# Kernel tuning notes

Hardware: AMD Instinct MI355X
Metric: run time of the kernel (lower is better)

Reference implementation:

```python
import jax, jax.numpy as jnp
import numpy as np

# geomloss SamplesLoss defaults for loss='sinkhorn'
BLUR = 0.05
SCALING = 0.5
P = 1  # norm=1 -> cost C(x,y) = ||x - y||_2


def _cost(x, y):
    # Euclidean distance cost (p=1). x:(B,N,D), y:(B,M,D) -> (B,N,M)
    d2 = (jnp.sum(x * x, -1)[:, :, None]
          - 2.0 * jnp.einsum('bnd,bmd->bnm', x, y)
          + jnp.sum(y * y, -1)[:, None, :])
    return jnp.sqrt(jnp.clip(d2, 1e-12, None))  # tiny clamp keeps sqrt grad finite on diagonal


def _softmin(eps, C, h):
    # f_i = -eps * logsumexp_j( h_j - C_ij / eps );  C:(B,N,M), h:(B,M) -> (B,N)
    return -eps * jax.nn.logsumexp(h[:, None, :] - C / eps, axis=2)


def _eps_schedule(diameter):
    # geomloss epsilon_schedule(p, diameter, blur, scaling)
    return ([diameter ** P]
            + [float(np.exp(e)) for e in np.arange(P * np.log(diameter), P * np.log(BLUR), P * np.log(SCALING))]
            + [BLUR ** P])


def _sinkhorn_divergence(x, y):
    # Debiased Sinkhorn divergence (geomloss, tensorized backend, balanced OT).
    B, N, D = x.shape
    M = y.shape[1]
    a_log = jnp.full((B, N), -np.log(N), dtype=x.dtype)  # uniform weights (log)
    b_log = jnp.full((B, M), -np.log(M), dtype=x.dtype)

    C_xy = _cost(x, y)
    C_yx = jnp.swapaxes(C_xy, 1, 2)  # symmetric cost
    C_xx = _cost(x, x)
    C_yy = _cost(y, y)

    # diameter of the joint point cloud (geomloss max_diameter); concrete python float
    xf = np.asarray(x).reshape(-1, D)
    yf = np.asarray(y).reshape(-1, D)
    mins = np.minimum(xf.min(0), yf.min(0))
    maxs = np.maximum(xf.max(0), yf.max(0))
    diameter = float(np.linalg.norm(maxs - mins))
    eps_list = _eps_schedule(diameter)

    sg = jax.lax.stop_gradient

    # initialization at the largest eps
    eps = eps_list[0]
    f_aa = _softmin(eps, C_xx, a_log)
    g_bb = _softmin(eps, C_yy, b_log)
    g_ab = _softmin(eps, C_yx, a_log)
    f_ba = _softmin(eps, C_xy, b_log)

    # epsilon-annealing loop with symmetric (averaged) updates; no grad flows
    # through this loop (outputs are stop_gradient'ed in the final extrapolation)
    for eps in eps_list:
        ft_ba = _softmin(eps, C_xy, b_log + g_ab / eps)
        gt_ab = _softmin(eps, C_yx, a_log + f_ba / eps)
        f_ba = 0.5 * (f_ba + ft_ba)
        g_ab = 0.5 * (g_ab + gt_ab)
        ft_aa = _softmin(eps, C_xx, a_log + f_aa / eps)
        gt_bb = _softmin(eps, C_yy, b_log + g_bb / eps)
        f_aa = 0.5 * (f_aa + ft_aa)
        g_bb = 0.5 * (g_bb + gt_bb)

    # last extrapolation at eps = blur^p with detached dual potentials (envelope theorem)
    eps = eps_list[-1]
    f_ba_new = _softmin(eps, C_xy, sg(b_log + g_ab / eps))
    g_ab_new = _softmin(eps, C_yx, sg(a_log + f_ba / eps))
    f_aa = _softmin(eps, C_xx, sg(a_log + f_aa / eps))
    g_bb = _softmin(eps, C_yy, sg(b_log + g_bb / eps))
    f_ba, g_ab = f_ba_new, g_ab_new

    a = jnp.exp(a_log)
    b = jnp.exp(b_log)
    # S_eps(a,b) = <a, f_ba - f_aa> + <b, g_ab - g_bb>, per batch element
    return jnp.sum(a * (f_ba - f_aa), -1) + jnp.sum(b * (g_ab - g_bb), -1)


def setup_inputs() -> dict:
    key = jax.random.key(0)
    k1, k2 = jax.random.split(key)
    pre = jax.random.normal(k1, (2, 4096, 2), dtype=jnp.float32)
    gt = jax.random.normal(k2, (2, 4096, 2), dtype=jnp.float32)
    return {"pre": pre, "gt": gt}


def reference(pre, gt):
    return _sinkhorn_divergence(pre, gt).mean()
```

## Files before the change

kernel.cpp:

```cpp
#include <hip/hip_runtime.h>
#include <math.h>

#define NPTS 4096
#define NB 2
#define K_TOTAL 12
#define BLOCK 256
#define TILE 128
#define NT (NPTS / TILE)

#define SCHED_OFF 0
#define ML_OFF 32
#define P_OFF 576
#define POT_SZ (4 * NB * NPTS)
#define PART_OFF (P_OFF + 2 * POT_SZ)
#define PART_SZ (4 * NB * NT * NPTS)

#if __has_builtin(__builtin_amdgcn_exp2f)
#define EXP2F __builtin_amdgcn_exp2f
#else
#define EXP2F exp2f
#endif
#if __has_builtin(__builtin_amdgcn_logf)
#define LOG2F __builtin_amdgcn_logf
#else
#define LOG2F log2f
#endif
#if __has_builtin(__builtin_amdgcn_sqrtf)
#define FSQRTF __builtin_amdgcn_sqrtf
#else
#define FSQRTF sqrtf
#endif

#define BASE_LOGW -8.31776616671934f
#define LOG2E 1.4426950408889634f
#define LN2 0.69314718055994531f

typedef float v2f __attribute__((ext_vector_type(2)));

__global__ __launch_bounds__(BLOCK) void k_init(
    const float2* __restrict__ x, const float2* __restrict__ y, float* ws)
{
  const int tid = threadIdx.x;
  const int bid = blockIdx.x;

  if (bid > 0) {
    for (int i = (bid - 1) * BLOCK + tid; i < 2 * POT_SZ; i += 63 * BLOCK)
      ws[P_OFF + i] = 0.0f;
    return;
  }

  float mnx = 1e30f, mny = 1e30f, mxx = -1e30f, mxy = -1e30f;
  for (int i = tid; i < NB * NPTS; i += BLOCK) {
    float2 p = x[i];
    mnx = fminf(mnx, p.x); mxx = fmaxf(mxx, p.x);
    mny = fminf(mny, p.y); mxy = fmaxf(mxy, p.y);
    float2 q = y[i];
    mnx = fminf(mnx, q.x); mxx = fmaxf(mxx, q.x);
    mny = fminf(mny, q.y); mxy = fmaxf(mxy, q.y);
  }
  for (int o = 32; o; o >>= 1) {
    mnx = fminf(mnx, __shfl_xor(mnx, o, 64));
    mxx = fmaxf(mxx, __shfl_xor(mxx, o, 64));
    mny = fminf(mny, __shfl_xor(mny, o, 64));
    mxy = fmaxf(mxy, __shfl_xor(mxy, o, 64));
  }
  __shared__ float r[4][4];
  const int wave = tid >> 6, lane = tid & 63;
  if (lane == 0) { r[0][wave] = mnx; r[1][wave] = mxx; r[2][wave] = mny; r[3][wave] = mxy; }
  __syncthreads();
  if (tid == 0) {
    mnx = fminf(fminf(r[0][0], r[0][1]), fminf(r[0][2], r[0][3]));
    mxx = fmaxf(fmaxf(r[1][0], r[1][1]), fmaxf(r[1][2], r[1][3]));
    mny = fminf(fminf(r[2][0], r[2][1]), fminf(r[2][2], r[2][3]));
    mxy = fmaxf(fmaxf(r[3][0], r[3][1]), fmaxf(r[3][2], r[3][3]));
    float rx = mxx - mnx, ry = mxy - mny;
    float dia = sqrtf(rx * rx + ry * ry);

    double a = log((double)dia);
    double stop = log(0.05);
    double stp = log(0.5);
    int cnt = (int)ceil((stop - a) / stp);
    if (cnt < 0) cnt = 0;
    if (cnt > K_TOTAL - 4) cnt = K_TOTAL - 4;

    float* sch = ws + SCHED_OFF;
    sch[0] = dia; sch[1] = 0.0f;
    sch[2] = dia; sch[3] = 0.5f;
    for (int k = 0; k < cnt; k++) {
      sch[2 * (2 + k)] = (float)exp(a + (double)k * stp);
      sch[2 * (2 + k) + 1] = 0.5f;
    }
    sch[2 * (2 + cnt)] = 0.05f; sch[2 * (2 + cnt) + 1] = 0.5f;
    for (int s = 3 + cnt; s < K_TOTAL - 1; s++) { sch[2 * s] = 0.05f; sch[2 * s + 1] = 1.0f; }
    sch[2 * (K_TOTAL - 1)] = 0.05f; sch[2 * (K_TOTAL - 1) + 1] = 0.0f;
  }
}

__global__ __launch_bounds__(BLOCK, 4) void k_tiles(
    const float2* __restrict__ xpts, const float2* __restrict__ ypts,
    float* __restrict__ ws, int stepi)
{
  __shared__ float rXs[TILE], rYs[TILE], rVs[TILE];
  __shared__ float cXs[144], cYs[144], cVs[144];
  __shared__ float tPart[16][129];
  __shared__ float sfb[2][32];
  __shared__ float smx[2];
  __shared__ float wmax[4];

  const int tid = threadIdx.x;
  const int id = blockIdx.x;

  const float2* rowp; const float2* colp;
  int ti, tj, pbr, pbc;
  bool dual;

  if (id < NB * NT * NT) {
    const int b = id >> 10;
    const int t = id & (NT * NT - 1);
    ti = t >> 5; tj = t & (NT - 1);
    rowp = xpts + b * NPTS; colp = ypts + b * NPTS;
    pbr = 0 * NB + b; pbc = 1 * NB + b;
    dual = true;
  } else {
    const int id2 = id - NB * NT * NT;
    const int mat = id2 / 1056;
    const int rem = id2 - mat * 1056;
    const int b = rem / 528;
    const int k = rem - b * 528;
    int t0 = (int)((65.0f - FSQRTF((float)(4225 - 8 * k))) * 0.5f);
    while (t0 * (65 - t0) / 2 > k) t0--;
    while ((t0 + 1) * (64 - t0) / 2 <= k) t0++;
    ti = t0; tj = t0 + (k - t0 * (65 - t0) / 2);
    const float2* pts = mat ? ypts : xpts;
    rowp = pts + b * NPTS; colp = rowp;
    pbr = (2 + mat) * NB + b; pbc = pbr;
    dual = (ti != tj);
  }

  const float eps = ws[SCHED_OFF + 2 * stepi];
  const float sc = LOG2E / eps;
  const float inv_eps = 1.0f / eps;
  const int ppar = (stepi - 1) & 1;
  const int cpar = stepi & 1;

  if (stepi > 0 && tid < 64) {
    const int c = tid & 31, side = tid >> 5;
    const int pb_own = side ? pbc : pbr;
    const int spb = (pb_own < 4) ? (pb_own ^ 2) : pb_own;
    float ml = ws[ML_OFF + ppar * 256 + spb * NT + c];
    float mm = ml;
    mm = fmaxf(mm, __shfl_xor(mm, 1, 64));
    mm = fmaxf(mm, __shfl_xor(mm, 2, 64));
    mm = fmaxf(mm, __shfl_xor(mm, 4, 64));
    mm = fmaxf(mm, __shfl_xor(mm, 8, 64));
    mm = fmaxf(mm, __shfl_xor(mm, 16, 64));
    sfb[side][c] = EXP2F((ml - mm) * LOG2E);
    if (c == 0) smx[side] = mm;
  }
  __syncthreads();

  const int side = tid >> 7, kk0 = tid & 127;
  const int pb_own = side ? pbc : pbr;
  const int tile_own = side ? tj : ti;
  const int r = tile_own * TILE + kk0;
  float2 pt = (side ? colp : rowp)[r];

  float h;
  if (stepi == 0) {
    h = BASE_LOGW;
  } else {
    const float eps_p = ws[SCHED_OFF + 2 * (stepi - 1)];
    const float w_p = ws[SCHED_OFF + 2 * (stepi - 1) + 1];
    const float* pprev = ws + PART_OFF + ppar * PART_SZ + (pb_own * NT) * NPTS + r;
    float s = 0.0f;
#pragma unroll
    for (int c = 0; c < NT; c++) s += pprev[c * NPTS] * sfb[side][c];
    s = fmaxf(s, 1e-37f);
    float ft = -eps_p * fmaf(LN2, LOG2F(s), smx[side]);
    float po = ws[P_OFF + cpar * POT_SZ + pb_own * NPTS + r];
    float pn = (w_p >= 1.0f) ? po : fmaf(w_p, po, (1.0f - w_p) * ft);
    ws[P_OFF + ppar * POT_SZ + pb_own * NPTS + r] = pn;
    h = fmaf(pn, inv_eps, BASE_LOGW);
  }

  float hm = h;
  for (int o = 32; o; o >>= 1) hm = fmaxf(hm, __shfl_xor(hm, o, 64));
  if ((tid & 63) == 0) wmax[tid >> 6] = hm;
  __syncthreads();
  const float Mloc = fmaxf(wmax[2 * side], wmax[2 * side + 1]);

  if (side == 0) {
    rXs[kk0] = pt.x * sc; rYs[kk0] = pt.y * sc;
    rVs[kk0] = EXP2F((h - Mloc) * LOG2E);
  } else {
    const int kk = kk0 + (kk0 >> 3);
    cXs[kk] = pt.x * sc; cYs[kk] = pt.y * sc;
    cVs[kk] = EXP2F((h - Mloc) * LOG2E);
  }
  if (kk0 == 0) ws[ML_OFF + cpar * 256 + pb_own * NT + tile_own] = Mloc;
  __syncthreads();

  const int tx = tid & 15, ty = tid >> 4;
  float rx[8], ry[8], rv[8];
  v2f cx2[4], cy2[4], cv2[4], racc2[8], cacc2[4];
#pragma unroll
  for (int q = 0; q < 8; q++) {
    rx[q] = rXs[ty * 8 + q]; ry[q] = rYs[ty * 8 + q]; rv[q] = rVs[ty * 8 + q];
    racc2[q] = (v2f){0.0f, 0.0f};
  }
#pragma unroll
  for (int j = 0; j < 4; j++) {
    const int ci = tx * 9 + 2 * j;
    cx2[j] = (v2f){cXs[ci], cXs[ci + 1]};
    cy2[j] = (v2f){cYs[ci], cYs[ci + 1]};
    cv2[j] = (v2f){cVs[ci], cVs[ci + 1]};
    cacc2[j] = (v2f){0.0f, 0.0f};
  }

#pragma unroll
  for (int q = 0; q < 8; q++) {
    const v2f rxq = (v2f){rx[q], rx[q]};
    const v2f ryq = (v2f){ry[q], ry[q]};
    const v2f rvq = (v2f){rv[q], rv[q]};
#pragma unroll
    for (int j = 0; j < 4; j++) {
      v2f dx = rxq - cx2[j];
      v2f dy = ryq - cy2[j];
      v2f d2 = dx * dx + dy * dy;
      float t0 = FSQRTF(d2.x), t1 = FSQRTF(d2.y);
      v2f K = (v2f){EXP2F(-t0), EXP2F(-t1)};
      racc2[q] += K * cv2[j];
      cacc2[j] += K * rvq;
    }
  }

  float* part = ws + PART_OFF + cpar * PART_SZ;

#pragma unroll
  for (int q = 0; q < 8; q++) tPart[tx][ty * 8 + q] = racc2[q].x + racc2[q].y;
  __syncthreads();
  if (tid < TILE) {
    float s = 0.0f;
#pragma unroll
    for (int t = 0; t < 16; t++) s += tPart[t][tid];
    part[(pbr * NT + tj) * NPTS + ti * TILE + tid] = s;
  }
  __syncthreads();

#pragma unroll
  for (int j = 0; j < 4; j++) {
    tPart[ty][tx * 8 + 2 * j] = cacc2[j].x;
    tPart[ty][tx * 8 + 2 * j + 1] = cacc2[j].y;
  }
  __syncthreads();
  if (dual && tid < TILE) {
    float s = 0.0f;
#pragma unroll
    for (int t = 0; t < 16; t++) s += tPart[t][tid];
    part[(pbc * NT + ti) * NPTS + tj * TILE + tid] = s;
  }
}

__global__ __launch_bounds__(1024) void k_reduce(const float* __restrict__ ws_c,
                                                 float* __restrict__ out)
{
  const float* ws = ws_c;
  const int tid = threadIdx.x;
  const int lpar = (K_TOTAL - 1) & 1;
  const float eps_l = ws[SCHED_OFF + 2 * (K_TOTAL - 1)];

  __shared__ float sfl[8][32];
  __shared__ float mm8[8];
  if (tid < 256) {
    const int g = tid >> 5, c = tid & 31;
    const int spb = (g < 4) ? (g ^ 2) : g;
    float ml = ws[ML_OFF + lpar * 256 + spb * NT + c];
    float mm = ml;
    mm = fmaxf(mm, __shfl_xor(mm, 1, 64));
    mm = fmaxf(mm, __shfl_xor(mm, 2, 64));
    mm = fmaxf(mm, __shfl_xor(mm, 4, 64));
    mm = fmaxf(mm, __shfl_xor(mm, 8, 64));
    mm = fmaxf(mm, __shfl_xor(mm, 16, 64));
    sfl[g][c] = EXP2F((ml - mm) * LOG2E);
    if (c == 0) mm8[g] = mm;
  }
  __syncthreads();

  double acc = 0.0;
  for (int idx = tid; idx < 4 * NB * NPTS; idx += 1024) {
    const int pb = idx >> 12, r = idx & (NPTS - 1);
    const float* pp = ws + PART_OFF + lpar * PART_SZ + (pb * NT) * NPTS + r;
    float s = 0.0f;
#pragma unroll
    for (int c = 0; c < NT; c++) s += pp[c * NPTS] * sfl[pb][c];
    s = fmaxf(s, 1e-37f);
    float f = -eps_l * fmaf(LN2, LOG2F(s), mm8[pb]);
    acc += (pb < 2 * NB) ? (double)f : -(double)f;
  }
  for (int o = 32; o; o >>= 1) acc += __shfl_xor(acc, o, 64);
  __shared__ double rd[16];
  const int wave = tid >> 6, lane = tid & 63;
  if (lane == 0) rd[wave] = acc;
  __syncthreads();
  if (tid == 0) {
    double s = 0.0;
#pragma unroll
    for (int i = 0; i < 16; i++) s += rd[i];
    out[0] = (float)(s / (double)(NB * NPTS));
  }
}

extern "C" void kernel_launch(void* const* d_in, const int* in_sizes, int n_in,
                              void* d_out, int out_size, void* d_ws, size_t ws_size,
                              hipStream_t stream)
{
  const float2* x = (const float2*)d_in[0];
  const float2* y = (const float2*)d_in[1];
  float* ws = (float*)d_ws;

  k_init<<<64, BLOCK, 0, stream>>>(x, y, ws);

  const int nblocks = NB * NT * NT + 2 * NB * (NT * (NT + 1)) / 2;
  for (int s = 0; s < K_TOTAL; s++) {
    k_tiles<<<nblocks, BLOCK, 0, stream>>>(x, y, ws, s);
  }
  k_reduce<<<1, 1024, 0, stream>>>(ws, (float*)d_out);
}
```

Before: 455.3 us.

## Double tile block threads, split partial-sum gather, and parallelize final reduction

The tile kernel now runs 512 threads per 128x128 tile. Each thread handles 8x4 pairs instead of 8x8, and the 32-way partial-sum gather is split across two threads joined with a shuffle. The single-block final reduction becomes a 64-block partial-sum kernel plus a tiny final kernel that writes doubles to a new workspace region. The aim is more parallelism and latency hiding per tile, at the cost of more register-file and LDS pressure per block and a larger cross-thread reduction (32 rows in tPart).

```diff
diff --git a/kernel.cpp b/kernel.cpp
--- a/kernel.cpp
+++ b/kernel.cpp
@@ -4,7 +4,7 @@
 #define NPTS 4096
 #define NB 2
 #define K_TOTAL 12
-#define BLOCK 256
+#define BLOCK 512
 #define TILE 128
 #define NT (NPTS / TILE)
 
@@ -12,7 +12,8 @@
 #define ML_OFF 32
 #define P_OFF 576
 #define POT_SZ (4 * NB * NPTS)
-#define PART_OFF (P_OFF + 2 * POT_SZ)
+#define RED_OFF (P_OFF + 2 * POT_SZ)
+#define PART_OFF (RED_OFF + 128)
 #define PART_SZ (4 * NB * NT * NPTS)
 
 #if __has_builtin(__builtin_amdgcn_exp2f)
@@ -37,20 +38,20 @@
 
 typedef float v2f __attribute__((ext_vector_type(2)));
 
-__global__ __launch_bounds__(BLOCK) void k_init(
+__global__ __launch_bounds__(256) void k_init(
     const float2* __restrict__ x, const float2* __restrict__ y, float* ws)
 {
   const int tid = threadIdx.x;
   const int bid = blockIdx.x;
 
   if (bid > 0) {
-    for (int i = (bid - 1) * BLOCK + tid; i < 2 * POT_SZ; i += 63 * BLOCK)
+    for (int i = (bid - 1) * 256 + tid; i < 2 * POT_SZ; i += 63 * 256)
       ws[P_OFF + i] = 0.0f;
     return;
   }
 
   float mnx = 1e30f, mny = 1e30f, mxx = -1e30f, mxy = -1e30f;
-  for (int i = tid; i < NB * NPTS; i += BLOCK) {
+  for (int i = tid; i < NB * NPTS; i += 256) {
     float2 p = x[i];
     mnx = fminf(mnx, p.x); mxx = fmaxf(mxx, p.x);
     mny = fminf(mny, p.y); mxy = fmaxf(mxy, p.y);
@@ -96,16 +97,16 @@
   }
 }
 
-__global__ __launch_bounds__(BLOCK, 4) void k_tiles(
+__global__ __launch_bounds__(BLOCK, 6) void k_tiles(
     const float2* __restrict__ xpts, const float2* __restrict__ ypts,
     float* __restrict__ ws, int stepi)
 {
   __shared__ float rXs[TILE], rYs[TILE], rVs[TILE];
   __shared__ float cXs[144], cYs[144], cVs[144];
-  __shared__ float tPart[16][129];
+  __shared__ float tPart[32][129];
   __shared__ float sfb[2][32];
   __shared__ float smx[2];
-  __shared__ float wmax[4];
+  __shared__ float wmax[8];
 
   const int tid = threadIdx.x;
   const int id = blockIdx.x;
@@ -144,8 +145,8 @@
   const int cpar = stepi & 1;
 
   if (stepi > 0 && tid < 64) {
-    const int c = tid & 31, side = tid >> 5;
-    const int pb_own = side ? pbc : pbr;
+    const int c = tid & 31, sd = tid >> 5;
+    const int pb_own = sd ? pbc : pbr;
     const int spb = (pb_own < 4) ? (pb_own ^ 2) : pb_own;
     float ml = ws[ML_OFF + ppar * 256 + spb * NT + c];
     float mm = ml;
@@ -154,12 +155,14 @@
     mm = fmaxf(mm, __shfl_xor(mm, 4, 64));
     mm = fmaxf(mm, __shfl_xor(mm, 8, 64));
     mm = fmaxf(mm, __shfl_xor(mm, 16, 64));
-    sfb[side][c] = EXP2F((ml - mm) * LOG2E);
-    if (c == 0) smx[side] = mm;
-  }
-  __syncthreads();
-
-  const int side = tid >> 7, kk0 = tid & 127;
+    sfb[sd][c] = EXP2F((ml - mm) * LOG2E);
+    if (c == 0) smx[sd] = mm;
+  }
+  __syncthreads();
+
+  const int p = tid >> 1, half = tid & 1;
+  const int side = tid >> 8;
+  const int kk0 = p & 127;
   const int pb_own = side ? pbc : pbr;
   const int tile_own = side ? tj : ti;
   const int r = tile_own * TILE + kk0;
@@ -174,12 +177,17 @@
     const float* pprev = ws + PART_OFF + ppar * PART_SZ + (pb_own * NT) * NPTS + r;
     float s = 0.0f;
 #pragma unroll
-    for (int c = 0; c < NT; c++) s += pprev[c * NPTS] * sfb[side][c];
+    for (int c = 0; c < 16; c++) {
+      const int cc = half * 16 + c;
+      s += pprev[cc * NPTS] * sfb[side][cc];
+    }
+    s += __shfl_xor(s, 1, 64);
     s = fmaxf(s, 1e-37f);
     float ft = -eps_p * fmaf(LN2, LOG2F(s), smx[side]);
     float po = ws[P_OFF + cpar * POT_SZ + pb_own * NPTS + r];
     float pn = (w_p >= 1.0f) ? po : fmaf(w_p, po, (1.0f - w_p) * ft);
-    ws[P_OFF + ppar * POT_SZ + pb_own * NPTS + r] = pn;
+    if (half == 0)
+      ws[P_OFF + ppar * POT_SZ + pb_own * NPTS + r] = pn;
     h = fmaf(pn, inv_eps, BASE_LOGW);
   }
 
@@ -187,30 +195,33 @@
   for (int o = 32; o; o >>= 1) hm = fmaxf(hm, __shfl_xor(hm, o, 64));
   if ((tid & 63) == 0) wmax[tid >> 6] = hm;
   __syncthreads();
-  const float Mloc = fmaxf(wmax[2 * side], wmax[2 * side + 1]);
-
-  if (side == 0) {
-    rXs[kk0] = pt.x * sc; rYs[kk0] = pt.y * sc;
-    rVs[kk0] = EXP2F((h - Mloc) * LOG2E);
-  } else {
-    const int kk = kk0 + (kk0 >> 3);
-    cXs[kk] = pt.x * sc; cYs[kk] = pt.y * sc;
-    cVs[kk] = EXP2F((h - Mloc) * LOG2E);
-  }
-  if (kk0 == 0) ws[ML_OFF + cpar * 256 + pb_own * NT + tile_own] = Mloc;
-  __syncthreads();
-
-  const int tx = tid & 15, ty = tid >> 4;
+  const float Mloc = fmaxf(fmaxf(wmax[side * 4 + 0], wmax[side * 4 + 1]),
+                           fmaxf(wmax[side * 4 + 2], wmax[side * 4 + 3]));
+
+  if (half == 0) {
+    const float V = EXP2F((h - Mloc) * LOG2E);
+    if (side == 0) {
+      rXs[kk0] = pt.x * sc; rYs[kk0] = pt.y * sc; rVs[kk0] = V;
+    } else {
+      const int kk = kk0 + (kk0 >> 3);
+      cXs[kk] = pt.x * sc; cYs[kk] = pt.y * sc; cVs[kk] = V;
+    }
+  }
+  if ((tid & 255) == 0)
+    ws[ML_OFF + cpar * 256 + pb_own * NT + tile_own] = Mloc;
+  __syncthreads();
+
+  const int tx = tid & 31, ty = tid >> 5;
   float rx[8], ry[8], rv[8];
-  v2f cx2[4], cy2[4], cv2[4], racc2[8], cacc2[4];
+  v2f cx2[2], cy2[2], cv2[2], racc2[8], cacc2[2];
 #pragma unroll
   for (int q = 0; q < 8; q++) {
     rx[q] = rXs[ty * 8 + q]; ry[q] = rYs[ty * 8 + q]; rv[q] = rVs[ty * 8 + q];
     racc2[q] = (v2f){0.0f, 0.0f};
   }
 #pragma unroll
-  for (int j = 0; j < 4; j++) {
-    const int ci = tx * 9 + 2 * j;
+  for (int j = 0; j < 2; j++) {
+    const int ci = tx * 4 + 2 * j + (tx >> 1);
     cx2[j] = (v2f){cXs[ci], cXs[ci + 1]};
     cy2[j] = (v2f){cYs[ci], cYs[ci + 1]};
     cv2[j] = (v2f){cVs[ci], cVs[ci + 1]};
@@ -223,7 +234,7 @@
     const v2f ryq = (v2f){ry[q], ry[q]};
     const v2f rvq = (v2f){rv[q], rv[q]};
 #pragma unroll
-    for (int j = 0; j < 4; j++) {
+    for (int j = 0; j < 2; j++) {
       v2f dx = rxq - cx2[j];
       v2f dy = ryq - cy2[j];
       v2f d2 = dx * dx + dy * dy;
@@ -242,16 +253,15 @@
   if (tid < TILE) {
     float s = 0.0f;
 #pragma unroll
-    for (int t = 0; t < 16; t++) s += tPart[t][tid];
+    for (int t = 0; t < 32; t++) s += tPart[t][tid];
     part[(pbr * NT + tj) * NPTS + ti * TILE + tid] = s;
   }
   __syncthreads();
 
-#pragma unroll
-  for (int j = 0; j < 4; j++) {
-    tPart[ty][tx * 8 + 2 * j] = cacc2[j].x;
-    tPart[ty][tx * 8 + 2 * j + 1] = cacc2[j].y;
-  }
+  tPart[ty][tx * 4 + 0] = cacc2[0].x;
+  tPart[ty][tx * 4 + 1] = cacc2[0].y;
+  tPart[ty][tx * 4 + 2] = cacc2[1].x;
+  tPart[ty][tx * 4 + 3] = cacc2[1].y;
   __syncthreads();
   if (dual && tid < TILE) {
     float s = 0.0f;
@@ -261,53 +271,57 @@
   }
 }
 
-__global__ __launch_bounds__(1024) void k_reduce(const float* __restrict__ ws_c,
-                                                 float* __restrict__ out)
-{
-  const float* ws = ws_c;
+__global__ __launch_bounds__(256) void k_psum(float* __restrict__ ws)
+{
+  const int pb = blockIdx.x >> 3, chunk = blockIdx.x & 7;
   const int tid = threadIdx.x;
   const int lpar = (K_TOTAL - 1) & 1;
   const float eps_l = ws[SCHED_OFF + 2 * (K_TOTAL - 1)];
 
-  __shared__ float sfl[8][32];
-  __shared__ float mm8[8];
-  if (tid < 256) {
-    const int g = tid >> 5, c = tid & 31;
-    const int spb = (g < 4) ? (g ^ 2) : g;
-    float ml = ws[ML_OFF + lpar * 256 + spb * NT + c];
+  __shared__ float sfl[32];
+  __shared__ float mmS;
+  if (tid < 32) {
+    const int spb = (pb < 4) ? (pb ^ 2) : pb;
+    float ml = ws[ML_OFF + lpar * 256 + spb * NT + tid];
     float mm = ml;
     mm = fmaxf(mm, __shfl_xor(mm, 1, 64));
     mm = fmaxf(mm, __shfl_xor(mm, 2, 64));
     mm = fmaxf(mm, __shfl_xor(mm, 4, 64));
     mm = fmaxf(mm, __shfl_xor(mm, 8, 64));
     mm = fmaxf(mm, __shfl_xor(mm, 16, 64));
-    sfl[g][c] = EXP2F((ml - mm) * LOG2E);
-    if (c == 0) mm8[g] = mm;
+    sfl[tid] = EXP2F((ml - mm) * LOG2E);
+    if (tid == 0) mmS = mm;
   }
   __syncthreads();
 
   double acc = 0.0;
-  for (int idx = tid; idx < 4 * NB * NPTS; idx += 1024) {
-    const int pb = idx >> 12, r = idx & (NPTS - 1);
+#pragma unroll
+  for (int rr = 0; rr < 2; rr++) {
+    const int r = chunk * 512 + rr * 256 + tid;
     const float* pp = ws + PART_OFF + lpar * PART_SZ + (pb * NT) * NPTS + r;
     float s = 0.0f;
 #pragma unroll
-    for (int c = 0; c < NT; c++) s += pp[c * NPTS] * sfl[pb][c];
+    for (int c = 0; c < NT; c++) s += pp[c * NPTS] * sfl[c];
     s = fmaxf(s, 1e-37f);
-    float f = -eps_l * fmaf(LN2, LOG2F(s), mm8[pb]);
-    acc += (pb < 2 * NB) ? (double)f : -(double)f;
+    float f = -eps_l * fmaf(LN2, LOG2F(s), mmS);
+    acc += (double)f;
   }
   for (int o = 32; o; o >>= 1) acc += __shfl_xor(acc, o, 64);
-  __shared__ double rd[16];
-  const int wave = tid >> 6, lane = tid & 63;
-  if (lane == 0) rd[wave] = acc;
+  __shared__ double rd[4];
+  if ((tid & 63) == 0) rd[tid >> 6] = acc;
   __syncthreads();
   if (tid == 0) {
-    double s = 0.0;
-#pragma unroll
-    for (int i = 0; i < 16; i++) s += rd[i];
-    out[0] = (float)(s / (double)(NB * NPTS));
-  }
+    double s = (rd[0] + rd[1]) + (rd[2] + rd[3]);
+    ((double*)(ws + RED_OFF))[blockIdx.x] = (pb < 2 * NB) ? s : -s;
+  }
+}
+
+__global__ __launch_bounds__(64) void k_final(const float* __restrict__ ws,
+                                              float* __restrict__ out)
+{
+  double v = ((const double*)(ws + RED_OFF))[threadIdx.x];
+  for (int o = 32; o; o >>= 1) v += __shfl_xor(v, o, 64);
+  if (threadIdx.x == 0) out[0] = (float)(v / (double)(NB * NPTS));
 }
 
 extern "C" void kernel_launch(void* const* d_in, const int* in_sizes, int n_in,
@@ -318,11 +332,12 @@
   const float2* y = (const float2*)d_in[1];
   float* ws = (float*)d_ws;
 
-  k_init<<<64, BLOCK, 0, stream>>>(x, y, ws);
+  k_init<<<64, 256, 0, stream>>>(x, y, ws);
 
   const int nblocks = NB * NT * NT + 2 * NB * (NT * (NT + 1)) / 2;
   for (int s = 0; s < K_TOTAL; s++) {
     k_tiles<<<nblocks, BLOCK, 0, stream>>>(x, y, ws, s);
   }
-  k_reduce<<<1, 1024, 0, stream>>>(ws, (float*)d_out);
-}
+  k_psum<<<64, 256, 0, stream>>>(ws);
+  k_final<<<1, 64, 0, stream>>>(ws, (float*)d_out);
+}
```

Measured after the change: 483.9 us. 1.06x slower.
